# Optimization experiments

Measured on AMD Instinct MI355X. Metric: run time of the kernel, lower is better.

## Reference

```python
import jax, jax.numpy as jnp
import numpy as np

B, S, D, H, O, E, K = 4, 2048, 1024, 2048, 1024, 8, 2

def setup_inputs() -> dict:
    key = jax.random.key(0)
    ks = jax.random.split(key, 8)
    x = jax.random.normal(ks[0], (B, S, D), dtype=jnp.float32)
    # kaiming-uniform-ish scale for weights, zero biases (as in _init_w)
    gate_w = jax.random.uniform(ks[1], (E, D), dtype=jnp.float32, minval=-1, maxval=1) * np.sqrt(6.0 / D)
    gate_b = jnp.zeros((E,), dtype=jnp.float32)
    w1 = jax.random.uniform(ks[2], (E, D, H), dtype=jnp.float32, minval=-1, maxval=1) * np.sqrt(6.0 / D)
    b1 = jnp.zeros((E, H), dtype=jnp.float32)
    w2 = jax.random.uniform(ks[3], (E, H, O), dtype=jnp.float32, minval=-1, maxval=1) * np.sqrt(6.0 / H)
    b2 = jnp.zeros((E, O), dtype=jnp.float32)
    return {"x": x, "gate_w": gate_w, "gate_b": gate_b, "w1": w1, "b1": b1, "w2": w2, "b2": b2}

def reference(x, gate_w, gate_b, w1, b1, w2, b2):
    # gate: softmax over experts, then top-k (k=2)
    logits = jnp.einsum('bsd,ed->bse', x, gate_w) + gate_b          # [B,S,E]
    probs = jax.nn.softmax(logits, axis=-1)
    topk_vals, topk_idx = jax.lax.top_k(probs, K)                    # [B,S,K]
    # dense all-expert MLPs (Linear-ReLU-Linear), dropout = 0
    h = jax.nn.relu(jnp.einsum('bsd,edh->bseh', x, w1) + b1)         # [B,S,E,H]
    expert_out = jnp.einsum('bseh,eho->bseo', h, w2) + b2            # [B,S,E,O]
    # gather top-k experts and combine with gate weights
    sel = jnp.take_along_axis(expert_out, topk_idx[..., None], axis=2)  # [B,S,K,O]
    return jnp.sum(sel * topk_vals[..., None], axis=2)               # [B,S,O]
```

## Files before the change

kernel.cpp:

```cpp
#include <hip/hip_runtime.h>

#define T_TOKENS 8192
#define D_DIM 1024
#define H_DIM 2048
#define O_DIM 1024
#define E_NUM 8
#define NPAIR 16384
#define GY_MAX 136

typedef unsigned short u16;
typedef __bf16 bf16x8 __attribute__((ext_vector_type(8)));
typedef float f32x4 __attribute__((ext_vector_type(4)));

#define VMCNT(n) asm volatile("s_waitcnt vmcnt(" #n ")" ::: "memory")

__device__ __forceinline__ void barsync() {
  asm volatile("" ::: "memory");
  __builtin_amdgcn_s_barrier();
  __builtin_amdgcn_sched_barrier(0);
}

__device__ inline u16 f2bf(float f) {
  union { float f; unsigned u; } v; v.f = f;
  unsigned r = v.u + 0x7FFFu + ((v.u >> 16) & 1u);
  return (u16)(r >> 16);
}

__device__ __forceinline__ void gload16(const u16* g, u16* l) {
  __builtin_amdgcn_global_load_lds((const __attribute__((address_space(1))) void*)g,
                                   (__attribute__((address_space(3))) void*)l, 16, 0, 0);
}

__global__ void transpose_cvt_kernel(const float* __restrict__ w, u16* __restrict__ wt,
                                     int R, int C) {
  __shared__ float tile[32][33];
  int e = blockIdx.z;
  int c0 = blockIdx.x * 32, r0 = blockIdx.y * 32;
  const float* wp = w + (size_t)e * R * C;
  u16* wtp = wt + (size_t)e * R * C;
  int tx = threadIdx.x, ty = threadIdx.y;
  #pragma unroll
  for (int j = 0; j < 32; j += 8)
    tile[ty + j][tx] = wp[(size_t)(r0 + ty + j) * C + c0 + tx];
  __syncthreads();
  #pragma unroll
  for (int j = 0; j < 32; j += 8)
    wtp[(size_t)(c0 + ty + j) * R + r0 + tx] = f2bf(tile[tx][ty + j]);
}

__global__ void gate_kernel(const float* __restrict__ x, const float* __restrict__ gw,
                            const float* __restrict__ gb, int* __restrict__ topk_idx,
                            float* __restrict__ topk_val, u16* __restrict__ xb) {
  int t = blockIdx.x * 4 + (threadIdx.x >> 6);
  int lane = threadIdx.x & 63;
  const float4* xr4 = (const float4*)(x + (size_t)t * D_DIM);
  const float4* gw4 = (const float4*)gw;
  u16* xbr = xb + (size_t)t * D_DIM;
  float acc[E_NUM];
  #pragma unroll
  for (int e = 0; e < E_NUM; e++) acc[e] = 0.f;
  #pragma unroll
  for (int it = 0; it < D_DIM / 256; ++it) {
    float4 xv = xr4[it * 64 + lane];
    ushort4 o;
    o.x = f2bf(xv.x); o.y = f2bf(xv.y); o.z = f2bf(xv.z); o.w = f2bf(xv.w);
    *(ushort4*)(xbr + (it * 64 + lane) * 4) = o;
    #pragma unroll
    for (int e = 0; e < E_NUM; e++) {
      float4 wv = gw4[e * (D_DIM / 4) + it * 64 + lane];
      acc[e] += xv.x * wv.x + xv.y * wv.y + xv.z * wv.z + xv.w * wv.w;
    }
  }
  #pragma unroll
  for (int e = 0; e < E_NUM; e++) {
    #pragma unroll
    for (int o = 32; o > 0; o >>= 1) acc[e] += __shfl_down(acc[e], o);
  }
  if (lane == 0) {
    float l[E_NUM], mx = -1e30f;
    #pragma unroll
    for (int e = 0; e < E_NUM; e++) { l[e] = acc[e] + gb[e]; mx = fmaxf(mx, l[e]); }
    float p[E_NUM], s = 0.f;
    #pragma unroll
    for (int e = 0; e < E_NUM; e++) { p[e] = expf(l[e] - mx); s += p[e]; }
    float inv = 1.f / s;
    int i1 = 0;
    #pragma unroll
    for (int e = 1; e < E_NUM; e++) if (p[e] > p[i1]) i1 = e;
    int i2 = (i1 == 0) ? 1 : 0;
    #pragma unroll
    for (int e = 0; e < E_NUM; e++) if (e != i1 && e != i2 && p[e] > p[i2]) i2 = e;
    topk_idx[t * 2] = i1;     topk_idx[t * 2 + 1] = i2;
    topk_val[t * 2] = p[i1] * inv; topk_val[t * 2 + 1] = p[i2] * inv;
  }
}

__global__ void histscan_kernel(const int* __restrict__ topk_idx,
                                int* __restrict__ counts, int* __restrict__ eoff,
                                int* __restrict__ nblk, int* __restrict__ tbl_e,
                                int* __restrict__ tbl_m0) {
  __shared__ int wh[4][E_NUM];
  int tid = threadIdx.x;
  int lane = tid & 63, wave = tid >> 6;
  int myc = 0;
  for (int i = tid; i < NPAIR; i += 256) {
    int e = topk_idx[i];
    #pragma unroll
    for (int ee = 0; ee < E_NUM; ee++) {
      unsigned long long m = __ballot(e == ee);
      if (lane == ee) myc += __popcll(m);
    }
  }
  if (lane < E_NUM) wh[wave][lane] = myc;
  __syncthreads();
  if (tid == 0) {
    int s = 0, cl[E_NUM];
    for (int e = 0; e < E_NUM; e++) {
      int c = wh[0][e] + wh[1][e] + wh[2][e] + wh[3][e];
      counts[e] = c;
      cl[e] = c;
      eoff[e] = s;
      s += c;
    }
    eoff[E_NUM] = s;
    int nb = 0;
    for (int e = 0; e < E_NUM; e++)
      for (int m0 = 0; m0 < cl[e]; m0 += 128) { tbl_e[nb] = e; tbl_m0[nb] = m0; nb++; }
    nblk[0] = nb;
  }
}

__global__ void scatter_kernel(const int* __restrict__ topk_idx, const float* __restrict__ topk_val,
                               const int* __restrict__ eoff, int* __restrict__ cursor_pad,
                               int* __restrict__ pair_token, int* __restrict__ inv_pos) {
  __shared__ int lhist[E_NUM];
  __shared__ int lbase[E_NUM];
  int tid = threadIdx.x;
  int t = blockIdx.x * 256 + tid;
  if (tid < E_NUM) lhist[tid] = 0;
  __syncthreads();
  int e0 = topk_idx[t * 2], e1 = topk_idx[t * 2 + 1];
  int r0 = atomicAdd(&lhist[e0], 1);
  int r1 = atomicAdd(&lhist[e1], 1);
  __syncthreads();
  if (tid < E_NUM) lbase[tid] = eoff[tid] + atomicAdd(&cursor_pad[tid * 32], lhist[tid]);
  __syncthreads();
  int p0 = lbase[e0] + r0;
  int p1 = lbase[e1] + r1;
  pair_token[p0] = t;
  pair_token[p1] = t;
  inv_pos[t * 2] = p0;
  inv_pos[t * 2 + 1] = p1;
}

__global__ void combine_kernel(const float* __restrict__ obuf, const int* __restrict__ inv_pos,
                               const float* __restrict__ topk_val, float* __restrict__ out) {
  int t = blockIdx.x;
  int tid = threadIdx.x;
  int p0 = inv_pos[t * 2], p1 = inv_pos[t * 2 + 1];
  float g0 = topk_val[t * 2], g1 = topk_val[t * 2 + 1];
  const float4* a4 = (const float4*)(obuf + (size_t)p0 * O_DIM);
  const float4* b4 = (const float4*)(obuf + (size_t)p1 * O_DIM);
  float4 a = a4[tid], b = b4[tid];
  float4 r;
  r.x = g0 * a.x + g1 * b.x;
  r.y = g0 * a.y + g1 * b.y;
  r.z = g0 * a.z + g1 * b.z;
  r.w = g0 * a.w + g1 * b.w;
  ((float4*)(out + (size_t)t * O_DIM))[tid] = r;
}


#define GEMM_DECLS                                                             \
  __shared__ __align__(16) u16 As0[4096], Bs0[4096], As1[4096], Bs1[4096],     \
      As2[4096], Bs2[4096];                                                    \
  const int tid = threadIdx.x;                                                 \
  const int wid = tid >> 6;                                                    \
  const int lane = tid & 63;                                                   \
  const int wm = (wid & 1) * 64;                                               \
  const int wn = (wid >> 1) * 64;                                              \
  const int lrow = lane & 15;                                                  \
  const int quad = lane >> 4;                                                  \
  f32x4 acc[4][4] = {};                                                        \
  auto STAGE = [&](u16* Ab, u16* Bb, int k0) {                                 \
    _Pragma("unroll")                                                          \
    for (int j = 0; j < 2; j++) {                                              \
      gload16(aptrA[j] + k0, Ab + (wid * 16 + j * 8) * 64);                    \
      gload16(bptrB[j] + k0, Bb + (wid * 16 + j * 8) * 64);                    \
    }                                                                          \
  };                                                                           \
  auto COMPUTE = [&](const u16* Ab, const u16* Bb) {                           \
    bf16x8 af[4], bfr[4];                                                      \
    _Pragma("unroll")                                                          \
    for (int i = 0; i < 4; i++) {                                              \
      int r = wm + i * 16 + lrow;                                              \
      int p = r >> 1;                                                          \
      int s = (((r & 1) << 2) | quad) ^ (p & 7);                               \
      af[i] = *(const bf16x8*)&Ab[p * 64 + s * 8];                             \
    }                                                                          \
    _Pragma("unroll")                                                          \
    for (int j = 0; j < 4; j++) {                                              \
      int r = wn + j * 16 + lrow;                                              \
      int p = r >> 1;                                                          \
      int s = (((r & 1) << 2) | quad) ^ (p & 7);                               \
      bfr[j] = *(const bf16x8*)&Bb[p * 64 + s * 8];                            \
    }                                                                          \
    __builtin_amdgcn_s_setprio(1);                                             \
    _Pragma("unroll")                                                          \
    for (int i = 0; i < 4; i++)                                                \
      _Pragma("unroll")                                                        \
      for (int j = 0; j < 4; j++)                                              \
        acc[i][j] = __builtin_amdgcn_mfma_f32_16x16x32_bf16(af[i], bfr[j],     \
                                                            acc[i][j], 0, 0, 0);\
    __builtin_amdgcn_s_setprio(0);                                             \
  }

__global__ __launch_bounds__(256, 3) void gemm1_kernel(
    const u16* __restrict__ xb, const u16* __restrict__ w1t, const float* __restrict__ b1,
    const int* __restrict__ pair_token, const int* __restrict__ eoff,
    const int* __restrict__ ecnt, const int* __restrict__ nblk,
    const int* __restrict__ tbl_e, const int* __restrict__ tbl_m0,
    u16* __restrict__ hbuf) {
  int lin = blockIdx.y * 16 + blockIdx.x;
  int swz = (lin & 7) * (16 * GY_MAX / 8) + (lin >> 3);
  const int bx = swz & 15;
  const int yb = swz >> 4;
  if (yb >= nblk[0]) return;
  const int e = tbl_e[yb];
  const int m0t = tbl_m0[yb];
  const int ne = ecnt[e];
  const int off = eoff[e];
  const int n0 = bx * 128;

  const u16* aptrA[2]; const u16* bptrB[2];
  {
    const int wid_ = threadIdx.x >> 6, lane_ = threadIdx.x & 63;
    #pragma unroll
    for (int j = 0; j < 2; j++) {
      int p = wid_ * 16 + j * 8 + (lane_ >> 3);
      int u = (lane_ & 7) ^ (p & 7);
      int r = 2 * p + (u >> 2);
      int c = u & 3;
      int gm = m0t + r;
      int tok = (gm < ne) ? pair_token[off + gm] : 0;
      aptrA[j] = xb + (size_t)tok * D_DIM + c * 8;
      bptrB[j] = w1t + ((size_t)e * H_DIM + (n0 + r)) * D_DIM + c * 8;
    }
  }

  GEMM_DECLS;

  STAGE(As0, Bs0, 0); STAGE(As1, Bs1, 32); STAGE(As2, Bs2, 64);
  #pragma unroll 1
  for (int t = 0; t <= 32 - 6; t += 3) {
    VMCNT(8); barsync(); COMPUTE(As0, Bs0); barsync(); STAGE(As0, Bs0, (t + 3) * 32);
    VMCNT(8); barsync(); COMPUTE(As1, Bs1); barsync(); STAGE(As1, Bs1, (t + 4) * 32);
    VMCNT(8); barsync(); COMPUTE(As2, Bs2); barsync(); STAGE(As2, Bs2, (t + 5) * 32);
  }
  VMCNT(8); barsync(); COMPUTE(As0, Bs0); barsync(); STAGE(As0, Bs0, 30 * 32);
  VMCNT(8); barsync(); COMPUTE(As1, Bs1); barsync(); STAGE(As1, Bs1, 31 * 32);
  VMCNT(8); barsync(); COMPUTE(As2, Bs2);
  VMCNT(4); barsync(); COMPUTE(As0, Bs0);
  VMCNT(0); barsync(); COMPUTE(As1, Bs1);

  #pragma unroll
  for (int i = 0; i < 4; i++) {
    #pragma unroll
    for (int r = 0; r < 4; r++) {
      int m = wm + i * 16 + quad * 4 + r;
      int gm = m0t + m;
      if (gm >= ne) continue;
      size_t rowbase = (size_t)(off + gm) * H_DIM;
      #pragma unroll
      for (int j = 0; j < 4; j++) {
        int n = n0 + wn + j * 16 + lrow;
        float v = acc[i][j][r] + b1[e * H_DIM + n];
        v = v > 0.f ? v : 0.f;
        hbuf[rowbase + n] = f2bf(v);
      }
    }
  }
}

__global__ __launch_bounds__(256, 3) void gemm2_kernel(
    const u16* __restrict__ hbuf, const u16* __restrict__ w2t, const float* __restrict__ b2,
    const int* __restrict__ eoff, const int* __restrict__ ecnt,
    const int* __restrict__ nblk, const int* __restrict__ tbl_e,
    const int* __restrict__ tbl_m0, float* __restrict__ obuf) {
  int lin = blockIdx.y * 8 + blockIdx.x;
  int swz = (lin & 7) * (8 * GY_MAX / 8) + (lin >> 3);
  const int bx = swz & 7;
  const int yb = swz >> 3;
  if (yb >= nblk[0]) return;
  const int e = tbl_e[yb];
  const int m0t = tbl_m0[yb];
  const int ne = ecnt[e];
  const int off = eoff[e];
  const int n0 = bx * 128;

  const u16* aptrA[2]; const u16* bptrB[2];
  {
    const int wid_ = threadIdx.x >> 6, lane_ = threadIdx.x & 63;
    #pragma unroll
    for (int j = 0; j < 2; j++) {
      int p = wid_ * 16 + j * 8 + (lane_ >> 3);
      int u = (lane_ & 7) ^ (p & 7);
      int r = 2 * p + (u >> 2);
      int c = u & 3;
      aptrA[j] = hbuf + (size_t)(off + m0t + r) * H_DIM + c * 8;
      bptrB[j] = w2t + ((size_t)e * O_DIM + (n0 + r)) * H_DIM + c * 8;
    }
  }

  GEMM_DECLS;

  STAGE(As0, Bs0, 0); STAGE(As1, Bs1, 32); STAGE(As2, Bs2, 64);
  #pragma unroll 1
  for (int t = 0; t <= 64 - 6; t += 3) {
    VMCNT(8); barsync(); COMPUTE(As0, Bs0); barsync(); STAGE(As0, Bs0, (t + 3) * 32);
    VMCNT(8); barsync(); COMPUTE(As1, Bs1); barsync(); STAGE(As1, Bs1, (t + 4) * 32);
    VMCNT(8); barsync(); COMPUTE(As2, Bs2); barsync(); STAGE(As2, Bs2, (t + 5) * 32);
  }
  VMCNT(8); barsync(); COMPUTE(As0, Bs0); barsync(); STAGE(As0, Bs0, 63 * 32);
  VMCNT(8); barsync(); COMPUTE(As1, Bs1);
  VMCNT(4); barsync(); COMPUTE(As2, Bs2);
  VMCNT(0); barsync(); COMPUTE(As0, Bs0);

  #pragma unroll
  for (int i = 0; i < 4; i++) {
    #pragma unroll
    for (int r = 0; r < 4; r++) {
      int m = wm + i * 16 + quad * 4 + r;
      int gm = m0t + m;
      if (gm >= ne) continue;
      size_t rowbase = (size_t)(off + gm) * O_DIM;
      #pragma unroll
      for (int j = 0; j < 4; j++) {
        int n = n0 + wn + j * 16 + lrow;
        obuf[rowbase + n] = acc[i][j][r] + b2[e * O_DIM + n];
      }
    }
  }
}

extern "C" void kernel_launch(void* const* d_in, const int* in_sizes, int n_in,
                              void* d_out, int out_size, void* d_ws, size_t ws_size,
                              hipStream_t stream) {
  const float* x  = (const float*)d_in[0];
  const float* gw = (const float*)d_in[1];
  const float* gb = (const float*)d_in[2];
  const float* w1 = (const float*)d_in[3];
  const float* b1 = (const float*)d_in[4];
  const float* w2 = (const float*)d_in[5];
  const float* b2 = (const float*)d_in[6];
  float* out = (float*)d_out;

  char* ws = (char*)d_ws;
  size_t off = 0;
  auto take = [&](size_t bytes) -> char* {
    char* p = ws + off;
    off = (off + bytes + 255) & ~(size_t)255;
    return p;
  };
  int*   meta       = (int*)take(4096);
  int*   cursor_pad = meta;
  int*   counts     = meta + 256;
  int*   eoff       = meta + 264;
  int*   nblk       = meta + 273;
  int*   tbl_e      = meta + 274;
  int*   tbl_m0     = meta + 410;
  int*   topk_idx   = (int*)take((size_t)T_TOKENS * 2 * 4);
  float* topk_val   = (float*)take((size_t)T_TOKENS * 2 * 4);
  int*   pair_token = (int*)take((size_t)(NPAIR + 256) * 4);
  int*   inv_pos    = (int*)take((size_t)T_TOKENS * 2 * 4);
  u16*   xb         = (u16*)take((size_t)T_TOKENS * D_DIM * 2);
  u16*   w1t        = (u16*)take((size_t)E_NUM * D_DIM * H_DIM * 2);
  u16*   w2t        = (u16*)take((size_t)E_NUM * H_DIM * O_DIM * 2);
  u16*   hbuf       = (u16*)take((size_t)(NPAIR + 128) * H_DIM * 2);
  float* obuf       = (float*)take((size_t)(NPAIR + 128) * O_DIM * 4);

  hipMemsetAsync(meta, 0, 4096, stream);

  transpose_cvt_kernel<<<dim3(H_DIM / 32, D_DIM / 32, E_NUM), dim3(32, 8), 0, stream>>>(w1, w1t, D_DIM, H_DIM);
  transpose_cvt_kernel<<<dim3(O_DIM / 32, H_DIM / 32, E_NUM), dim3(32, 8), 0, stream>>>(w2, w2t, H_DIM, O_DIM);
  gate_kernel<<<T_TOKENS / 4, 256, 0, stream>>>(x, gw, gb, topk_idx, topk_val, xb);
  histscan_kernel<<<1, 256, 0, stream>>>(topk_idx, counts, eoff, nblk, tbl_e, tbl_m0);
  scatter_kernel<<<T_TOKENS / 256, 256, 0, stream>>>(topk_idx, topk_val, eoff, cursor_pad, pair_token, inv_pos);
  gemm1_kernel<<<dim3(16, GY_MAX), 256, 0, stream>>>(xb, w1t, b1, pair_token, eoff, counts, nblk, tbl_e, tbl_m0, hbuf);
  gemm2_kernel<<<dim3(8, GY_MAX), 256, 0, stream>>>(hbuf, w2t, b2, eoff, counts, nblk, tbl_e, tbl_m0, obuf);
  combine_kernel<<<T_TOKENS, 256, 0, stream>>>(obuf, inv_pos, topk_val, out);
}
```

Before: 451.5 us.

## Replace triple-buffered GEMM pipeline with single-buffer BK=64 loop and larger transpose tiles

The grouped expert GEMMs drop the three-stage LDS ring with explicit vmcnt waits and move to one 128x64 LDS tile per operand. Each step loads the tile, syncs, runs two k-halves of MFMA, then syncs again, and the swizzle layout changes to match. Less LDS per block allows launch bounds of 4 blocks per CU, but global-load latency is no longer hidden behind compute within a block. The weight transpose-convert kernel also moves to 64x64 tiles with 64x4 threads.

```diff
diff --git a/kernel.cpp b/kernel.cpp
--- a/kernel.cpp
+++ b/kernel.cpp
@@ -12,14 +12,6 @@
 typedef __bf16 bf16x8 __attribute__((ext_vector_type(8)));
 typedef float f32x4 __attribute__((ext_vector_type(4)));
 
-#define VMCNT(n) asm volatile("s_waitcnt vmcnt(" #n ")" ::: "memory")
-
-__device__ __forceinline__ void barsync() {
-  asm volatile("" ::: "memory");
-  __builtin_amdgcn_s_barrier();
-  __builtin_amdgcn_sched_barrier(0);
-}
-
 __device__ inline u16 f2bf(float f) {
   union { float f; unsigned u; } v; v.f = f;
   unsigned r = v.u + 0x7FFFu + ((v.u >> 16) & 1u);
@@ -33,18 +25,18 @@
 
 __global__ void transpose_cvt_kernel(const float* __restrict__ w, u16* __restrict__ wt,
                                      int R, int C) {
-  __shared__ float tile[32][33];
+  __shared__ float tile[64][65];
   int e = blockIdx.z;
-  int c0 = blockIdx.x * 32, r0 = blockIdx.y * 32;
+  int c0 = blockIdx.x * 64, r0 = blockIdx.y * 64;
   const float* wp = w + (size_t)e * R * C;
   u16* wtp = wt + (size_t)e * R * C;
   int tx = threadIdx.x, ty = threadIdx.y;
   #pragma unroll
-  for (int j = 0; j < 32; j += 8)
+  for (int j = 0; j < 64; j += 4)
     tile[ty + j][tx] = wp[(size_t)(r0 + ty + j) * C + c0 + tx];
   __syncthreads();
   #pragma unroll
-  for (int j = 0; j < 32; j += 8)
+  for (int j = 0; j < 64; j += 4)
     wtp[(size_t)(c0 + ty + j) * R + r0 + tx] = f2bf(tile[tx][ty + j]);
 }
 
@@ -172,50 +164,55 @@
 
 
 #define GEMM_DECLS                                                             \
-  __shared__ __align__(16) u16 As0[4096], Bs0[4096], As1[4096], Bs1[4096],     \
-      As2[4096], Bs2[4096];                                                    \
+  __shared__ __align__(16) u16 As[128 * 64];                                   \
+  __shared__ __align__(16) u16 Bs[128 * 64];                                   \
   const int tid = threadIdx.x;                                                 \
   const int wid = tid >> 6;                                                    \
   const int lane = tid & 63;                                                   \
+  const int strow8 = lane >> 3;                                                \
+  const int slot = lane & 7;                                                   \
   const int wm = (wid & 1) * 64;                                               \
   const int wn = (wid >> 1) * 64;                                              \
   const int lrow = lane & 15;                                                  \
   const int quad = lane >> 4;                                                  \
+  const int pg0 = quad ^ (lrow & 7);                                           \
+  const int pg1 = (quad + 4) ^ (lrow & 7);                                     \
   f32x4 acc[4][4] = {};                                                        \
-  auto STAGE = [&](u16* Ab, u16* Bb, int k0) {                                 \
-    _Pragma("unroll")                                                          \
-    for (int j = 0; j < 2; j++) {                                              \
-      gload16(aptrA[j] + k0, Ab + (wid * 16 + j * 8) * 64);                    \
-      gload16(bptrB[j] + k0, Bb + (wid * 16 + j * 8) * 64);                    \
-    }                                                                          \
-  };                                                                           \
-  auto COMPUTE = [&](const u16* Ab, const u16* Bb) {                           \
-    bf16x8 af[4], bfr[4];                                                      \
-    _Pragma("unroll")                                                          \
-    for (int i = 0; i < 4; i++) {                                              \
-      int r = wm + i * 16 + lrow;                                              \
-      int p = r >> 1;                                                          \
-      int s = (((r & 1) << 2) | quad) ^ (p & 7);                               \
-      af[i] = *(const bf16x8*)&Ab[p * 64 + s * 8];                             \
-    }                                                                          \
+  auto KTILE = [&](int k0) {                                                   \
     _Pragma("unroll")                                                          \
     for (int j = 0; j < 4; j++) {                                              \
-      int r = wn + j * 16 + lrow;                                              \
-      int p = r >> 1;                                                          \
-      int s = (((r & 1) << 2) | quad) ^ (p & 7);                               \
-      bfr[j] = *(const bf16x8*)&Bb[p * 64 + s * 8];                            \
+      gload16(aptr[j] + k0, As + wid * 2048 + j * 512);                        \
+      gload16(bptr[j] + k0, Bs + wid * 2048 + j * 512);                        \
     }                                                                          \
-    __builtin_amdgcn_s_setprio(1);                                             \
-    _Pragma("unroll")                                                          \
-    for (int i = 0; i < 4; i++)                                                \
-      _Pragma("unroll")                                                        \
-      for (int j = 0; j < 4; j++)                                              \
-        acc[i][j] = __builtin_amdgcn_mfma_f32_16x16x32_bf16(af[i], bfr[j],     \
-                                                            acc[i][j], 0, 0, 0);\
-    __builtin_amdgcn_s_setprio(0);                                             \
-  }
-
-__global__ __launch_bounds__(256, 3) void gemm1_kernel(
+    __syncthreads();                                                           \
+    {                                                                          \
+      bf16x8 af[4], bfr[4];                                                    \
+      _Pragma("unroll")                                                        \
+      for (int i = 0; i < 4; i++) af[i] = *(const bf16x8*)&As[(wm + i * 16 + lrow) * 64 + pg0 * 8]; \
+      _Pragma("unroll")                                                        \
+      for (int j = 0; j < 4; j++) bfr[j] = *(const bf16x8*)&Bs[(wn + j * 16 + lrow) * 64 + pg0 * 8]; \
+      _Pragma("unroll")                                                        \
+      for (int i = 0; i < 4; i++)                                              \
+        _Pragma("unroll")                                                      \
+        for (int j = 0; j < 4; j++)                                            \
+          acc[i][j] = __builtin_amdgcn_mfma_f32_16x16x32_bf16(af[i], bfr[j], acc[i][j], 0, 0, 0); \
+    }                                                                          \
+    {                                                                          \
+      bf16x8 af[4], bfr[4];                                                    \
+      _Pragma("unroll")                                                        \
+      for (int i = 0; i < 4; i++) af[i] = *(const bf16x8*)&As[(wm + i * 16 + lrow) * 64 + pg1 * 8]; \
+      _Pragma("unroll")                                                        \
+      for (int j = 0; j < 4; j++) bfr[j] = *(const bf16x8*)&Bs[(wn + j * 16 + lrow) * 64 + pg1 * 8]; \
+      _Pragma("unroll")                                                        \
+      for (int i = 0; i < 4; i++)                                              \
+        _Pragma("unroll")                                                      \
+        for (int j = 0; j < 4; j++)                                            \
+          acc[i][j] = __builtin_amdgcn_mfma_f32_16x16x32_bf16(af[i], bfr[j], acc[i][j], 0, 0, 0); \
+    }                                                                          \
+    __syncthreads();                                                           \
+  }
+
+__global__ __launch_bounds__(256, 4) void gemm1_kernel(
     const u16* __restrict__ xb, const u16* __restrict__ w1t, const float* __restrict__ b1,
     const int* __restrict__ pair_token, const int* __restrict__ eoff,
     const int* __restrict__ ecnt, const int* __restrict__ nblk,
@@ -232,36 +229,23 @@
   const int off = eoff[e];
   const int n0 = bx * 128;
 
-  const u16* aptrA[2]; const u16* bptrB[2];
+  const u16* aptr[4]; const u16* bptr[4];
   {
     const int wid_ = threadIdx.x >> 6, lane_ = threadIdx.x & 63;
     #pragma unroll
-    for (int j = 0; j < 2; j++) {
-      int p = wid_ * 16 + j * 8 + (lane_ >> 3);
-      int u = (lane_ & 7) ^ (p & 7);
-      int r = 2 * p + (u >> 2);
-      int c = u & 3;
+    for (int j = 0; j < 4; j++) {
+      int r = wid_ * 32 + j * 8 + (lane_ >> 3);
       int gm = m0t + r;
       int tok = (gm < ne) ? pair_token[off + gm] : 0;
-      aptrA[j] = xb + (size_t)tok * D_DIM + c * 8;
-      bptrB[j] = w1t + ((size_t)e * H_DIM + (n0 + r)) * D_DIM + c * 8;
+      int gl = (lane_ & 7) ^ (r & 7);
+      aptr[j] = xb + (size_t)tok * D_DIM + gl * 8;
+      bptr[j] = w1t + ((size_t)e * H_DIM + (n0 + r)) * D_DIM + gl * 8;
     }
   }
 
   GEMM_DECLS;
 
-  STAGE(As0, Bs0, 0); STAGE(As1, Bs1, 32); STAGE(As2, Bs2, 64);
-  #pragma unroll 1
-  for (int t = 0; t <= 32 - 6; t += 3) {
-    VMCNT(8); barsync(); COMPUTE(As0, Bs0); barsync(); STAGE(As0, Bs0, (t + 3) * 32);
-    VMCNT(8); barsync(); COMPUTE(As1, Bs1); barsync(); STAGE(As1, Bs1, (t + 4) * 32);
-    VMCNT(8); barsync(); COMPUTE(As2, Bs2); barsync(); STAGE(As2, Bs2, (t + 5) * 32);
-  }
-  VMCNT(8); barsync(); COMPUTE(As0, Bs0); barsync(); STAGE(As0, Bs0, 30 * 32);
-  VMCNT(8); barsync(); COMPUTE(As1, Bs1); barsync(); STAGE(As1, Bs1, 31 * 32);
-  VMCNT(8); barsync(); COMPUTE(As2, Bs2);
-  VMCNT(4); barsync(); COMPUTE(As0, Bs0);
-  VMCNT(0); barsync(); COMPUTE(As1, Bs1);
+  for (int k0 = 0; k0 < D_DIM; k0 += 64) KTILE(k0);
 
   #pragma unroll
   for (int i = 0; i < 4; i++) {
@@ -282,7 +266,7 @@
   }
 }
 
-__global__ __launch_bounds__(256, 3) void gemm2_kernel(
+__global__ __launch_bounds__(256, 4) void gemm2_kernel(
     const u16* __restrict__ hbuf, const u16* __restrict__ w2t, const float* __restrict__ b2,
     const int* __restrict__ eoff, const int* __restrict__ ecnt,
     const int* __restrict__ nblk, const int* __restrict__ tbl_e,
@@ -298,33 +282,21 @@
   const int off = eoff[e];
   const int n0 = bx * 128;
 
-  const u16* aptrA[2]; const u16* bptrB[2];
+  const u16* aptr[4]; const u16* bptr[4];
   {
     const int wid_ = threadIdx.x >> 6, lane_ = threadIdx.x & 63;
     #pragma unroll
-    for (int j = 0; j < 2; j++) {
-      int p = wid_ * 16 + j * 8 + (lane_ >> 3);
-      int u = (lane_ & 7) ^ (p & 7);
-      int r = 2 * p + (u >> 2);
-      int c = u & 3;
-      aptrA[j] = hbuf + (size_t)(off + m0t + r) * H_DIM + c * 8;
-      bptrB[j] = w2t + ((size_t)e * O_DIM + (n0 + r)) * H_DIM + c * 8;
+    for (int j = 0; j < 4; j++) {
+      int r = wid_ * 32 + j * 8 + (lane_ >> 3);
+      int gl = (lane_ & 7) ^ (r & 7);
+      aptr[j] = hbuf + (size_t)(off + m0t + r) * H_DIM + gl * 8;
+      bptr[j] = w2t + ((size_t)e * O_DIM + (n0 + r)) * H_DIM + gl * 8;
     }
   }
 
   GEMM_DECLS;
 
-  STAGE(As0, Bs0, 0); STAGE(As1, Bs1, 32); STAGE(As2, Bs2, 64);
-  #pragma unroll 1
-  for (int t = 0; t <= 64 - 6; t += 3) {
-    VMCNT(8); barsync(); COMPUTE(As0, Bs0); barsync(); STAGE(As0, Bs0, (t + 3) * 32);
-    VMCNT(8); barsync(); COMPUTE(As1, Bs1); barsync(); STAGE(As1, Bs1, (t + 4) * 32);
-    VMCNT(8); barsync(); COMPUTE(As2, Bs2); barsync(); STAGE(As2, Bs2, (t + 5) * 32);
-  }
-  VMCNT(8); barsync(); COMPUTE(As0, Bs0); barsync(); STAGE(As0, Bs0, 63 * 32);
-  VMCNT(8); barsync(); COMPUTE(As1, Bs1);
-  VMCNT(4); barsync(); COMPUTE(As2, Bs2);
-  VMCNT(0); barsync(); COMPUTE(As0, Bs0);
+  for (int k0 = 0; k0 < H_DIM; k0 += 64) KTILE(k0);
 
   #pragma unroll
   for (int i = 0; i < 4; i++) {
@@ -381,8 +353,8 @@
 
   hipMemsetAsync(meta, 0, 4096, stream);
 
-  transpose_cvt_kernel<<<dim3(H_DIM / 32, D_DIM / 32, E_NUM), dim3(32, 8), 0, stream>>>(w1, w1t, D_DIM, H_DIM);
-  transpose_cvt_kernel<<<dim3(O_DIM / 32, H_DIM / 32, E_NUM), dim3(32, 8), 0, stream>>>(w2, w2t, H_DIM, O_DIM);
+  transpose_cvt_kernel<<<dim3(H_DIM / 64, D_DIM / 64, E_NUM), dim3(64, 4), 0, stream>>>(w1, w1t, D_DIM, H_DIM);
+  transpose_cvt_kernel<<<dim3(O_DIM / 64, H_DIM / 64, E_NUM), dim3(64, 4), 0, stream>>>(w2, w2t, H_DIM, O_DIM);
   gate_kernel<<<T_TOKENS / 4, 256, 0, stream>>>(x, gw, gb, topk_idx, topk_val, xb);
   histscan_kernel<<<1, 256, 0, stream>>>(topk_idx, counts, eoff, nblk, tbl_e, tbl_m0);
   scatter_kernel<<<T_TOKENS / 256, 256, 0, stream>>>(topk_idx, topk_val, eoff, cursor_pad, pair_token, inv_pos);
```

Result: slower. 587.9 us (+30.2%).

## Drop histscan kernel and merge weight transposes to cut launches

Applied to the files above, without the earlier changes.

Merges the two weight transpose-convert launches into one flat-grid kernel. Moves the per-expert counting into the gate kernel via global atomics and removes the single-block histogram/scan kernel. The scatter kernel now derives expert offsets by prefix-summing the counts, and the GEMM kernels walk the counts to find their expert and row tile, replacing the precomputed tables. This removes one serial single-block kernel and one launch, at the cost of contended global atomics in the gate kernel and a small per-block loop in the GEMMs.

```diff
diff --git a/kernel.cpp b/kernel.cpp
--- a/kernel.cpp
+++ b/kernel.cpp
@@ -31,13 +31,24 @@
                                    (__attribute__((address_space(3))) void*)l, 16, 0, 0);
 }
 
-__global__ void transpose_cvt_kernel(const float* __restrict__ w, u16* __restrict__ wt,
-                                     int R, int C) {
+__global__ void transpose_cvt_all(const float* __restrict__ w1, u16* __restrict__ w1t,
+                                  const float* __restrict__ w2, u16* __restrict__ w2t) {
   __shared__ float tile[32][33];
-  int e = blockIdx.z;
-  int c0 = blockIdx.x * 32, r0 = blockIdx.y * 32;
-  const float* wp = w + (size_t)e * R * C;
-  u16* wtp = wt + (size_t)e * R * C;
+  int bid = blockIdx.x;
+  const float* wp; u16* wtp; int R, C, bx, by;
+  if (bid < 16384) {
+    int e = bid >> 11, t = bid & 2047;
+    bx = t & 63; by = t >> 6;
+    R = D_DIM; C = H_DIM;
+    wp = w1 + (size_t)e * R * C; wtp = w1t + (size_t)e * R * C;
+  } else {
+    int r = bid - 16384;
+    int e = r >> 11, t = r & 2047;
+    bx = t & 31; by = t >> 5;
+    R = H_DIM; C = O_DIM;
+    wp = w2 + (size_t)e * R * C; wtp = w2t + (size_t)e * R * C;
+  }
+  int c0 = bx * 32, r0 = by * 32;
   int tx = threadIdx.x, ty = threadIdx.y;
   #pragma unroll
   for (int j = 0; j < 32; j += 8)
@@ -50,7 +61,8 @@
 
 __global__ void gate_kernel(const float* __restrict__ x, const float* __restrict__ gw,
                             const float* __restrict__ gb, int* __restrict__ topk_idx,
-                            float* __restrict__ topk_val, u16* __restrict__ xb) {
+                            float* __restrict__ topk_val, u16* __restrict__ xb,
+                            int* __restrict__ counts_pad) {
   int t = blockIdx.x * 4 + (threadIdx.x >> 6);
   int lane = threadIdx.x & 63;
   const float4* xr4 = (const float4*)(x + (size_t)t * D_DIM);
@@ -92,46 +104,13 @@
     for (int e = 0; e < E_NUM; e++) if (e != i1 && e != i2 && p[e] > p[i2]) i2 = e;
     topk_idx[t * 2] = i1;     topk_idx[t * 2 + 1] = i2;
     topk_val[t * 2] = p[i1] * inv; topk_val[t * 2 + 1] = p[i2] * inv;
-  }
-}
-
-__global__ void histscan_kernel(const int* __restrict__ topk_idx,
-                                int* __restrict__ counts, int* __restrict__ eoff,
-                                int* __restrict__ nblk, int* __restrict__ tbl_e,
-                                int* __restrict__ tbl_m0) {
-  __shared__ int wh[4][E_NUM];
-  int tid = threadIdx.x;
-  int lane = tid & 63, wave = tid >> 6;
-  int myc = 0;
-  for (int i = tid; i < NPAIR; i += 256) {
-    int e = topk_idx[i];
-    #pragma unroll
-    for (int ee = 0; ee < E_NUM; ee++) {
-      unsigned long long m = __ballot(e == ee);
-      if (lane == ee) myc += __popcll(m);
-    }
-  }
-  if (lane < E_NUM) wh[wave][lane] = myc;
-  __syncthreads();
-  if (tid == 0) {
-    int s = 0, cl[E_NUM];
-    for (int e = 0; e < E_NUM; e++) {
-      int c = wh[0][e] + wh[1][e] + wh[2][e] + wh[3][e];
-      counts[e] = c;
-      cl[e] = c;
-      eoff[e] = s;
-      s += c;
-    }
-    eoff[E_NUM] = s;
-    int nb = 0;
-    for (int e = 0; e < E_NUM; e++)
-      for (int m0 = 0; m0 < cl[e]; m0 += 128) { tbl_e[nb] = e; tbl_m0[nb] = m0; nb++; }
-    nblk[0] = nb;
-  }
-}
-
-__global__ void scatter_kernel(const int* __restrict__ topk_idx, const float* __restrict__ topk_val,
-                               const int* __restrict__ eoff, int* __restrict__ cursor_pad,
+    atomicAdd(&counts_pad[i1 * 32], 1);
+    atomicAdd(&counts_pad[i2 * 32], 1);
+  }
+}
+
+__global__ void scatter_kernel(const int* __restrict__ topk_idx,
+                               const int* __restrict__ counts_pad, int* __restrict__ cursor_pad,
                                int* __restrict__ pair_token, int* __restrict__ inv_pos) {
   __shared__ int lhist[E_NUM];
   __shared__ int lbase[E_NUM];
@@ -143,7 +122,11 @@
   int r0 = atomicAdd(&lhist[e0], 1);
   int r1 = atomicAdd(&lhist[e1], 1);
   __syncthreads();
-  if (tid < E_NUM) lbase[tid] = eoff[tid] + atomicAdd(&cursor_pad[tid * 32], lhist[tid]);
+  if (tid < E_NUM) {
+    int s = 0;
+    for (int ee = 0; ee < tid; ee++) s += counts_pad[ee * 32];
+    lbase[tid] = s + atomicAdd(&cursor_pad[tid * 32], lhist[tid]);
+  }
   __syncthreads();
   int p0 = lbase[e0] + r0;
   int p1 = lbase[e1] + r1;
@@ -171,6 +154,20 @@
 }
 
 
+#define TILE_WALK(YB, E_, M0_, NE_, OFF_)                                      \
+  int E_ = 0, M0_ = -1, NE_ = 0, OFF_ = 0;                                     \
+  {                                                                            \
+    int nb = 0, s = 0;                                                         \
+    _Pragma("unroll")                                                          \
+    for (int ee = 0; ee < E_NUM; ee++) {                                       \
+      int c = counts_pad[ee * 32];                                             \
+      int tt = (c + 127) >> 7;                                                 \
+      if (M0_ < 0 && (YB) < nb + tt) { E_ = ee; M0_ = ((YB) - nb) << 7; NE_ = c; OFF_ = s; } \
+      nb += tt; s += c;                                                        \
+    }                                                                          \
+  }                                                                            \
+  if (M0_ < 0) return
+
 #define GEMM_DECLS                                                             \
   __shared__ __align__(16) u16 As0[4096], Bs0[4096], As1[4096], Bs1[4096],     \
       As2[4096], Bs2[4096];                                                    \
@@ -217,19 +214,13 @@
 
 __global__ __launch_bounds__(256, 3) void gemm1_kernel(
     const u16* __restrict__ xb, const u16* __restrict__ w1t, const float* __restrict__ b1,
-    const int* __restrict__ pair_token, const int* __restrict__ eoff,
-    const int* __restrict__ ecnt, const int* __restrict__ nblk,
-    const int* __restrict__ tbl_e, const int* __restrict__ tbl_m0,
+    const int* __restrict__ pair_token, const int* __restrict__ counts_pad,
     u16* __restrict__ hbuf) {
   int lin = blockIdx.y * 16 + blockIdx.x;
   int swz = (lin & 7) * (16 * GY_MAX / 8) + (lin >> 3);
   const int bx = swz & 15;
   const int yb = swz >> 4;
-  if (yb >= nblk[0]) return;
-  const int e = tbl_e[yb];
-  const int m0t = tbl_m0[yb];
-  const int ne = ecnt[e];
-  const int off = eoff[e];
+  TILE_WALK(yb, e, m0t, ne, off);
   const int n0 = bx * 128;
 
   const u16* aptrA[2]; const u16* bptrB[2];
@@ -284,18 +275,12 @@
 
 __global__ __launch_bounds__(256, 3) void gemm2_kernel(
     const u16* __restrict__ hbuf, const u16* __restrict__ w2t, const float* __restrict__ b2,
-    const int* __restrict__ eoff, const int* __restrict__ ecnt,
-    const int* __restrict__ nblk, const int* __restrict__ tbl_e,
-    const int* __restrict__ tbl_m0, float* __restrict__ obuf) {
+    const int* __restrict__ counts_pad, float* __restrict__ obuf) {
   int lin = blockIdx.y * 8 + blockIdx.x;
   int swz = (lin & 7) * (8 * GY_MAX / 8) + (lin >> 3);
   const int bx = swz & 7;
   const int yb = swz >> 3;
-  if (yb >= nblk[0]) return;
-  const int e = tbl_e[yb];
-  const int m0t = tbl_m0[yb];
-  const int ne = ecnt[e];
-  const int off = eoff[e];
+  TILE_WALK(yb, e, m0t, ne, off);
   const int n0 = bx * 128;
 
   const u16* aptrA[2]; const u16* bptrB[2];
@@ -364,11 +349,7 @@
   };
   int*   meta       = (int*)take(4096);
   int*   cursor_pad = meta;
-  int*   counts     = meta + 256;
-  int*   eoff       = meta + 264;
-  int*   nblk       = meta + 273;
-  int*   tbl_e      = meta + 274;
-  int*   tbl_m0     = meta + 410;
+  int*   counts_pad = meta + 256;
   int*   topk_idx   = (int*)take((size_t)T_TOKENS * 2 * 4);
   float* topk_val   = (float*)take((size_t)T_TOKENS * 2 * 4);
   int*   pair_token = (int*)take((size_t)(NPAIR + 256) * 4);
@@ -381,12 +362,10 @@
 
   hipMemsetAsync(meta, 0, 4096, stream);
 
-  transpose_cvt_kernel<<<dim3(H_DIM / 32, D_DIM / 32, E_NUM), dim3(32, 8), 0, stream>>>(w1, w1t, D_DIM, H_DIM);
-  transpose_cvt_kernel<<<dim3(O_DIM / 32, H_DIM / 32, E_NUM), dim3(32, 8), 0, stream>>>(w2, w2t, H_DIM, O_DIM);
-  gate_kernel<<<T_TOKENS / 4, 256, 0, stream>>>(x, gw, gb, topk_idx, topk_val, xb);
-  histscan_kernel<<<1, 256, 0, stream>>>(topk_idx, counts, eoff, nblk, tbl_e, tbl_m0);
-  scatter_kernel<<<T_TOKENS / 256, 256, 0, stream>>>(topk_idx, topk_val, eoff, cursor_pad, pair_token, inv_pos);
-  gemm1_kernel<<<dim3(16, GY_MAX), 256, 0, stream>>>(xb, w1t, b1, pair_token, eoff, counts, nblk, tbl_e, tbl_m0, hbuf);
-  gemm2_kernel<<<dim3(8, GY_MAX), 256, 0, stream>>>(hbuf, w2t, b2, eoff, counts, nblk, tbl_e, tbl_m0, obuf);
+  transpose_cvt_all<<<dim3(32768), dim3(32, 8), 0, stream>>>(w1, w1t, w2, w2t);
+  gate_kernel<<<T_TOKENS / 4, 256, 0, stream>>>(x, gw, gb, topk_idx, topk_val, xb, counts_pad);
+  scatter_kernel<<<T_TOKENS / 256, 256, 0, stream>>>(topk_idx, counts_pad, cursor_pad, pair_token, inv_pos);
+  gemm1_kernel<<<dim3(16, GY_MAX), 256, 0, stream>>>(xb, w1t, b1, pair_token, counts_pad, hbuf);
+  gemm2_kernel<<<dim3(8, GY_MAX), 256, 0, stream>>>(hbuf, w2t, b2, counts_pad, obuf);
   combine_kernel<<<T_TOKENS, 256, 0, stream>>>(obuf, inv_pos, topk_val, out);
 }
```

Result: faster. 433.5 us (-4.0%).
